# Performance work log

Measured on AMD Instinct MI355X. Metric: run time of the kernel, lower is better.

## Reference

```python
import jax, jax.numpy as jnp
import numpy as np

EPS = 1e-6
SIGMA = 0.02  # inverse-quadratic kernel scale (RGBuvHistBlock default)
H_BINS = 128


def _rgb_uv_hist(x, mu):
    # x: [B, 3, H, W] in [0, 1]; mu: [h] bin centers in [-3, 3]
    x = jnp.clip(x, 0.0, 1.0)
    B = x.shape[0]
    I = x.reshape(B, 3, -1)                       # [B, 3, N]
    Iy = jnp.sqrt(jnp.sum(I * I, axis=1) + EPS)   # [B, N] intensity scaling
    logI = jnp.log(I + EPS)                       # [B, 3, N]

    def kern(d):
        # inverse-quadratic kernel: 1 / (1 + (|d| / sigma)^2)
        return 1.0 / (1.0 + (d / SIGMA) ** 2)

    def chan(c0, c1, c2):
        Iu = logI[:, c0] - logI[:, c1]            # [B, N]
        Iv = logI[:, c0] - logI[:, c2]            # [B, N]
        du = kern(jnp.abs(Iu[:, :, None] - mu[None, None, :]))  # [B, N, h]
        dv = kern(jnp.abs(Iv[:, :, None] - mu[None, None, :]))  # [B, N, h]
        a = Iy[:, :, None] * du                   # [B, N, h]
        return jnp.einsum('bnu,bnv->buv', a, dv)  # [B, h, h]

    # channel order: r vs (g,b), g vs (r,b), b vs (r,g)
    hists = jnp.stack([chan(0, 1, 2), chan(1, 0, 2), chan(2, 0, 1)], axis=1)  # [B,3,h,h]
    norm = jnp.sum(hists, axis=(1, 2, 3)).reshape(-1, 1, 1, 1) + EPS
    return hists / norm


def setup_inputs() -> dict:
    key = jax.random.key(0)
    k1, k2 = jax.random.split(key)
    B, C, H, W = 4, 3, 256, 256
    pred = jax.random.uniform(k1, (B, C, H, W), dtype=jnp.float32)
    target = jax.random.uniform(k2, (B, C, H, W), dtype=jnp.float32)
    return {"pred": pred, "target": target}


def reference(pred, target):
    mu = jnp.linspace(-3.0, 3.0, H_BINS, dtype=pred.dtype)
    pred_hist = _rgb_uv_hist(pred, mu)
    target_hist = _rgb_uv_hist(target, mu)
    diff = jnp.sqrt(target_hist) - jnp.sqrt(pred_hist)
    return (1.0 / np.sqrt(2.0)) * jnp.sqrt(jnp.sum(diff * diff)) / pred_hist.shape[0]
```

## Files before the change

kernel.cpp:

```cpp
#include <hip/hip_runtime.h>

#define NPIX   65536
#define HB     128
#define EPSF   1e-6f
#define ROWB   80
#define MATB   (HB * ROWB)
#define BUFB   (3 * MATB)
#define PPW    24576
#define NCHUNK 32

typedef _Float16 half8  __attribute__((ext_vector_type(8)));
typedef __fp16   fp16x2 __attribute__((ext_vector_type(2)));
typedef float    f32x16 __attribute__((ext_vector_type(16)));
typedef float    f32x2  __attribute__((ext_vector_type(2)));

__device__ __forceinline__ unsigned pk2(float a, float b) {
    union { fp16x2 h; unsigned u; } cv;
    cv.h = __builtin_amdgcn_cvt_pkrtz(a, b);
    return cv.u;
}

__global__ __launch_bounds__(512, 2) void hist_mfma(
    const float* __restrict__ pred, const float* __restrict__ tgt,
    unsigned* __restrict__ parts, float* __restrict__ norms, int nchunk)
{
    __shared__ char smat[2 * BUFB];
    __shared__ float wsum[8];

    const int t    = threadIdx.x;
    const int lane = t & 63;
    const int wave = t >> 6;
    const int chunk = blockIdx.x % nchunk;
    const int ib    = blockIdx.x / nchunk;
    const int b     = ib & 3;
    const int img   = ib >> 2;
    const int kchunk = NPIX / nchunk;
    const int nreg   = kchunk >> 5;

    const float* __restrict__ base = (img ? tgt : pred) + (size_t)b * 3 * NPIX;
    const float* __restrict__ Rp = base;
    const float* __restrict__ Gp = base + NPIX;
    const float* __restrict__ Bp = base + 2 * NPIX;

    const int   i16     = t & 15;
    const int   rbase   = t >> 4;
    const float MU0     = (float)rbase * (300.0f / 127.0f) - 150.0f;
    const float MUSTEP  = 32.0f * (300.0f / 127.0f);
    char* genp0 = smat + rbase * ROWB + i16 * 4;
    char* genp1 = genp0 + BUFB;

    const int wu = wave >> 2;
    const int wv = wave & 3;
    const int la = lane & 31;

    f32x16 acc[3][2];
#pragma unroll
    for (int g = 0; g < 3; ++g)
#pragma unroll
        for (int i = 0; i < 2; ++i)
#pragma unroll
            for (int r = 0; r < 16; ++r) acc[g][i][r] = 0.0f;

    const int n0 = chunk * kchunk;

    f32x2 Ra, Ga, Ba, Rb, Gb, Bb;
    f32x2 ddrg, ddrb, ddgb, rw2;

    auto issue_ld = [&](int reg, f32x2& R, f32x2& G, f32x2& B) {
        const int n = n0 + reg * 32 + 2 * i16;
        R = *reinterpret_cast<const f32x2*>(Rp + n);
        G = *reinterpret_cast<const f32x2*>(Gp + n);
        B = *reinterpret_cast<const f32x2*>(Bp + n);
    };

    auto scalars = [&](f32x2 R, f32x2 G, f32x2 B) {
        const float C = 34.65735902799726547086f;
        float r0 = fminf(fmaxf(R.x, 0.0f), 1.0f);
        float r1 = fminf(fmaxf(R.y, 0.0f), 1.0f);
        float g0 = fminf(fmaxf(G.x, 0.0f), 1.0f);
        float g1 = fminf(fmaxf(G.y, 0.0f), 1.0f);
        float b0 = fminf(fmaxf(B.x, 0.0f), 1.0f);
        float b1 = fminf(fmaxf(B.y, 0.0f), 1.0f);
        float lr0 = __builtin_amdgcn_logf(r0 + EPSF);
        float lr1 = __builtin_amdgcn_logf(r1 + EPSF);
        float lg0 = __builtin_amdgcn_logf(g0 + EPSF);
        float lg1 = __builtin_amdgcn_logf(g1 + EPSF);
        float lb0 = __builtin_amdgcn_logf(b0 + EPSF);
        float lb1 = __builtin_amdgcn_logf(b1 + EPSF);
        ddrg.x = (lr0 - lg0) * C;  ddrg.y = (lr1 - lg1) * C;
        ddrb.x = (lr0 - lb0) * C;  ddrb.y = (lr1 - lb1) * C;
        ddgb.x = (lg0 - lb0) * C;  ddgb.y = (lg1 - lb1) * C;
        const float s0 = __builtin_fmaf(r0, r0,
                          __builtin_fmaf(g0, g0,
                           __builtin_fmaf(b0, b0, EPSF)));
        const float s1 = __builtin_fmaf(r1, r1,
                          __builtin_fmaf(g1, g1,
                           __builtin_fmaf(b1, b1, EPSF)));
        rw2.x = __builtin_amdgcn_sqrtf(__builtin_amdgcn_sqrtf(s0));
        rw2.y = __builtin_amdgcn_sqrtf(__builtin_amdgcn_sqrtf(s1));
    };

    auto gen_mat = [&](char* bp, int mat, f32x2 dd) {
        float m = MU0;
#pragma unroll
        for (int s = 0; s < 4; ++s) {
            const float ex = dd.x - m, ey = dd.y - m;
            const float tx = __builtin_fmaf(ex, ex, 1.0f);
            const float ty = __builtin_fmaf(ey, ey, 1.0f);
            const float vx = __builtin_amdgcn_rcpf(tx) * rw2.x;
            const float vy = __builtin_amdgcn_rcpf(ty) * rw2.y;
            *reinterpret_cast<unsigned*>(bp + mat * MATB + s * 32 * ROWB)
                = pk2(vx, vy);
            m += MUSTEP;
        }
    };

    auto rd = [&](const char* mp, int matid, int row, int koff) -> half8 {
        return *reinterpret_cast<const half8*>(mp + matid * MATB
                                               + row * ROWB + koff);
    };

    auto body = [&](const char* mp, char* gp, bool dogen) {
        const int kbase = (lane >> 5) << 4;
        const int r0 = wu * 64 + la;
        const int c0 = wv * 32 + la;

        if (dogen) gen_mat(gp, 0, ddrg);
        {
            half8 a0 = rd(mp, 0, r0,      kbase);
            half8 a1 = rd(mp, 0, r0 + 32, kbase);
            half8 p  = rd(mp, 1, c0,      kbase);
            __builtin_amdgcn_s_setprio(1);
            acc[0][0] = __builtin_amdgcn_mfma_f32_32x32x16_f16(a0, p, acc[0][0], 0, 0, 0);
            acc[0][1] = __builtin_amdgcn_mfma_f32_32x32x16_f16(a1, p, acc[0][1], 0, 0, 0);
            __builtin_amdgcn_s_setprio(0);

            if (dogen) gen_mat(gp, 1, ddrb);
            half8 q   = rd(mp, 2, c0,      kbase);
            half8 bb0 = rd(mp, 1, r0,      kbase);
            half8 bb1 = rd(mp, 1, r0 + 32, kbase);
            __builtin_amdgcn_s_setprio(1);
            acc[1][0] = __builtin_amdgcn_mfma_f32_32x32x16_f16(a0, q, acc[1][0], 0, 0, 0);
            acc[1][1] = __builtin_amdgcn_mfma_f32_32x32x16_f16(a1, q, acc[1][1], 0, 0, 0);
            acc[2][0] = __builtin_amdgcn_mfma_f32_32x32x16_f16(bb0, q, acc[2][0], 0, 0, 0);
            acc[2][1] = __builtin_amdgcn_mfma_f32_32x32x16_f16(bb1, q, acc[2][1], 0, 0, 0);
            __builtin_amdgcn_s_setprio(0);
        }

        if (dogen) gen_mat(gp, 2, ddgb);
        {
            const int k1 = 32 + kbase;
            half8 a0  = rd(mp, 0, r0,      k1);
            half8 a1  = rd(mp, 0, r0 + 32, k1);
            half8 p   = rd(mp, 1, c0,      k1);
            half8 q   = rd(mp, 2, c0,      k1);
            half8 bb0 = rd(mp, 1, r0,      k1);
            half8 bb1 = rd(mp, 1, r0 + 32, k1);
            __builtin_amdgcn_s_setprio(1);
            acc[0][0] = __builtin_amdgcn_mfma_f32_32x32x16_f16(a0, p, acc[0][0], 0, 0, 0);
            acc[0][1] = __builtin_amdgcn_mfma_f32_32x32x16_f16(a1, p, acc[0][1], 0, 0, 0);
            acc[1][0] = __builtin_amdgcn_mfma_f32_32x32x16_f16(a0, q, acc[1][0], 0, 0, 0);
            acc[1][1] = __builtin_amdgcn_mfma_f32_32x32x16_f16(a1, q, acc[1][1], 0, 0, 0);
            acc[2][0] = __builtin_amdgcn_mfma_f32_32x32x16_f16(bb0, q, acc[2][0], 0, 0, 0);
            acc[2][1] = __builtin_amdgcn_mfma_f32_32x32x16_f16(bb1, q, acc[2][1], 0, 0, 0);
            __builtin_amdgcn_s_setprio(0);
        }
    };

    issue_ld(0, Ra, Ga, Ba);
    scalars(Ra, Ga, Ba);
    gen_mat(genp0, 0, ddrg);
    gen_mat(genp0, 1, ddrb);
    gen_mat(genp0, 2, ddgb);
    issue_ld(1, Rb, Gb, Bb);
    __syncthreads();

    for (int rg = 0; rg < nreg; rg += 2) {
        scalars(Rb, Gb, Bb);
        issue_ld(min(rg + 2, nreg - 1), Ra, Ga, Ba);
        body(smat, genp1, true);
        __syncthreads();
        scalars(Ra, Ga, Ba);
        issue_ld(min(rg + 3, nreg - 1), Rb, Gb, Bb);
        body(smat + BUFB, genp0, rg + 2 < nreg);
        __syncthreads();
    }

    unsigned* pb0 = parts + (size_t)blockIdx.x * PPW;
    float blksum = 0.0f;
#pragma unroll
    for (int g = 0; g < 3; ++g)
#pragma unroll
        for (int i2 = 0; i2 < 2; ++i2) {
            unsigned* wp = pb0
                + (size_t)(((g * 8 + wave) * 2 + i2) * 8) * 64 + lane;
#pragma unroll
            for (int rh = 0; rh < 8; ++rh) {
                wp[rh * 64] = pk2(acc[g][i2][2 * rh], acc[g][i2][2 * rh + 1]);
                blksum += acc[g][i2][2 * rh] + acc[g][i2][2 * rh + 1];
            }
        }

    for (int o = 32; o > 0; o >>= 1) blksum += __shfl_down(blksum, o, 64);
    if (lane == 0) wsum[wave] = blksum;
    __syncthreads();
    if (t == 0) {
        float s = 0.0f;
#pragma unroll
        for (int w = 0; w < 8; ++w) s += wsum[w];
        atomicAdd(&norms[ib], s);
    }
}

__global__ __launch_bounds__(256) void reduce_loss(
    const unsigned* __restrict__ parts, const float* __restrict__ norms,
    float* __restrict__ acc, int nchunk)
{
    const int i      = blockIdx.x * 256 + threadIdx.x;
    const int comb12 = i >> 13;
    const int rest   = i & 8191;
    const int b      = comb12 / 3;
    const int g      = comb12 % 3;
    const unsigned* pp = parts + (size_t)(b * nchunk) * PPW + g * 8192 + rest;
    const unsigned* pt = parts + (size_t)((4 + b) * nchunk) * PPW + g * 8192 + rest;

    float hp0 = 0.0f, hp1 = 0.0f, ht0 = 0.0f, ht1 = 0.0f;
    int k = 0;
    for (; k + 8 <= nchunk; k += 8) {
#pragma unroll
        for (int j = 0; j < 8; ++j) {
            union { unsigned u; fp16x2 h; } a, c;
            a.u = pp[(size_t)(k + j) * PPW];
            c.u = pt[(size_t)(k + j) * PPW];
            hp0 += (float)a.h.x;  hp1 += (float)a.h.y;
            ht0 += (float)c.h.x;  ht1 += (float)c.h.y;
        }
    }
    for (; k < nchunk; ++k) {
        union { unsigned u; fp16x2 h; } a, c;
        a.u = pp[(size_t)k * PPW];
        c.u = pt[(size_t)k * PPW];
        hp0 += (float)a.h.x;  hp1 += (float)a.h.y;
        ht0 += (float)c.h.x;  ht1 += (float)c.h.y;
    }

    const float rp = __builtin_amdgcn_rcpf(norms[b] + EPSF);
    const float rt = __builtin_amdgcn_rcpf(norms[4 + b] + EPSF);
    const float d0 = __builtin_amdgcn_sqrtf(ht0 * rt)
                   - __builtin_amdgcn_sqrtf(hp0 * rp);
    const float d1 = __builtin_amdgcn_sqrtf(ht1 * rt)
                   - __builtin_amdgcn_sqrtf(hp1 * rp);
    float s = __builtin_fmaf(d0, d0, d1 * d1);
    for (int o = 32; o > 0; o >>= 1) s += __shfl_down(s, o, 64);
    __shared__ float wsum[4];
    if ((threadIdx.x & 63) == 0) wsum[threadIdx.x >> 6] = s;
    __syncthreads();
    if (threadIdx.x == 0) atomicAdd(acc, wsum[0] + wsum[1] + wsum[2] + wsum[3]);
}

__global__ void final_k(const float* __restrict__ acc, float* __restrict__ out)
{
    out[0] = __builtin_amdgcn_sqrtf(acc[0]) * 0.70710678118654752440f * 0.25f;
}

extern "C" void kernel_launch(void* const* d_in, const int* in_sizes, int n_in,
                              void* d_out, int out_size, void* d_ws, size_t ws_size,
                              hipStream_t stream)
{
    const float* pred = (const float*)d_in[0];
    const float* tgt  = (const float*)d_in[1];
    float* ws  = (float*)d_ws;
    float* out = (float*)d_out;

    float*    norms = ws;
    float*    acc   = ws + 8;
    unsigned* parts = (unsigned*)(ws + 16);

    int nchunk = NCHUNK;
    while (nchunk > 1) {
        const size_t need = (16 + (size_t)8 * nchunk * PPW) * sizeof(float);
        if (need <= ws_size) break;
        nchunk >>= 1;
    }

    (void)hipMemsetAsync(ws, 0, 9 * sizeof(float), stream);

    hist_mfma<<<8 * nchunk, 512, 0, stream>>>(pred, tgt, parts, norms, nchunk);
    reduce_loss<<<12 * 8192 / 256, 256, 0, stream>>>(parts, norms, acc, nchunk);
    final_k<<<1, 1, 0, stream>>>(acc, out);
}
```

Baseline: 100.9 us.

## Split work across 12 waves with one histogram per wave group

The block grows from 512 to 768 threads. Each group of 256 threads now generates only one of the three kernel matrices, and each group of four waves computes a full 128x128 histogram as 2x2 tiles of 64x64. Each thread takes two log calls instead of six and writes eight rows instead of twelve, and every wave issues four MFMAs per k-step with plain A/B fragment reuse. The cost is more waves per block, a different register budget under launch_bounds(768,3), and a new output layout in the partial buffer that the reduce kernel must still index correctly.

```diff
diff --git a/kernel.cpp b/kernel.cpp
--- a/kernel.cpp
+++ b/kernel.cpp
@@ -20,12 +20,12 @@
     return cv.u;
 }
 
-__global__ __launch_bounds__(512, 2) void hist_mfma(
+__global__ __launch_bounds__(768, 3) void hist_mfma(
     const float* __restrict__ pred, const float* __restrict__ tgt,
     unsigned* __restrict__ parts, float* __restrict__ norms, int nchunk)
 {
     __shared__ char smat[2 * BUFB];
-    __shared__ float wsum[8];
+    __shared__ float wsum[12];
 
     const int t    = threadIdx.x;
     const int lane = t & 63;
@@ -42,29 +42,35 @@
     const float* __restrict__ Gp = base + NPIX;
     const float* __restrict__ Bp = base + 2 * NPIX;
 
-    const int   i16     = t & 15;
-    const int   rbase   = t >> 4;
+    const int   mat     = t >> 8;
+    const int   tp      = t & 255;
+    const int   i16     = tp & 15;
+    const int   rbase   = tp >> 4;
     const float MU0     = (float)rbase * (300.0f / 127.0f) - 150.0f;
-    const float MUSTEP  = 32.0f * (300.0f / 127.0f);
-    char* genp0 = smat + rbase * ROWB + i16 * 4;
+    const float MUSTEP  = 16.0f * (300.0f / 127.0f);
+    char* genp0 = smat + mat * MATB + rbase * ROWB + i16 * 4;
     char* genp1 = genp0 + BUFB;
 
-    const int wu = wave >> 2;
-    const int wv = wave & 3;
-    const int la = lane & 31;
-
-    f32x16 acc[3][2];
-#pragma unroll
-    for (int g = 0; g < 3; ++g)
-#pragma unroll
-        for (int i = 0; i < 2; ++i)
-#pragma unroll
-            for (int r = 0; r < 16; ++r) acc[g][i][r] = 0.0f;
+    const int g    = wave >> 2;
+    const int i2   = (wave >> 1) & 1;
+    const int j2   = wave & 1;
+    const int Amat = (g == 2) ? 1 : 0;
+    const int Bmat = (g == 0) ? 1 : 2;
+    const int la   = lane & 31;
+    const int kb16 = (lane >> 5) << 4;
+    const int arow = i2 * 64 + la;
+    const int brow = j2 * 64 + la;
+
+    f32x16 acc[4];
+#pragma unroll
+    for (int i = 0; i < 4; ++i)
+#pragma unroll
+        for (int r = 0; r < 16; ++r) acc[i][r] = 0.0f;
 
     const int n0 = chunk * kchunk;
 
     f32x2 Ra, Ga, Ba, Rb, Gb, Bb;
-    f32x2 ddrg, ddrb, ddgb, rw2;
+    f32x2 dd, rw2;
 
     auto issue_ld = [&](int reg, f32x2& R, f32x2& G, f32x2& B) {
         const int n = n0 + reg * 32 + 2 * i16;
@@ -81,15 +87,14 @@
         float g1 = fminf(fmaxf(G.y, 0.0f), 1.0f);
         float b0 = fminf(fmaxf(B.x, 0.0f), 1.0f);
         float b1 = fminf(fmaxf(B.y, 0.0f), 1.0f);
-        float lr0 = __builtin_amdgcn_logf(r0 + EPSF);
-        float lr1 = __builtin_amdgcn_logf(r1 + EPSF);
-        float lg0 = __builtin_amdgcn_logf(g0 + EPSF);
-        float lg1 = __builtin_amdgcn_logf(g1 + EPSF);
-        float lb0 = __builtin_amdgcn_logf(b0 + EPSF);
-        float lb1 = __builtin_amdgcn_logf(b1 + EPSF);
-        ddrg.x = (lr0 - lg0) * C;  ddrg.y = (lr1 - lg1) * C;
-        ddrb.x = (lr0 - lb0) * C;  ddrb.y = (lr1 - lb1) * C;
-        ddgb.x = (lg0 - lb0) * C;  ddgb.y = (lg1 - lb1) * C;
+        const float x0a = (mat == 2) ? g0 : r0;
+        const float x1a = (mat == 2) ? g1 : r1;
+        const float y0a = (mat == 0) ? g0 : b0;
+        const float y1a = (mat == 0) ? g1 : b1;
+        dd.x = (__builtin_amdgcn_logf(x0a + EPSF)
+              - __builtin_amdgcn_logf(y0a + EPSF)) * C;
+        dd.y = (__builtin_amdgcn_logf(x1a + EPSF)
+              - __builtin_amdgcn_logf(y1a + EPSF)) * C;
         const float s0 = __builtin_fmaf(r0, r0,
                           __builtin_fmaf(g0, g0,
                            __builtin_fmaf(b0, b0, EPSF)));
@@ -100,106 +105,69 @@
         rw2.y = __builtin_amdgcn_sqrtf(__builtin_amdgcn_sqrtf(s1));
     };
 
-    auto gen_mat = [&](char* bp, int mat, f32x2 dd) {
+    auto gen = [&](char* bp) {
         float m = MU0;
 #pragma unroll
-        for (int s = 0; s < 4; ++s) {
+        for (int s = 0; s < 8; ++s) {
             const float ex = dd.x - m, ey = dd.y - m;
             const float tx = __builtin_fmaf(ex, ex, 1.0f);
             const float ty = __builtin_fmaf(ey, ey, 1.0f);
             const float vx = __builtin_amdgcn_rcpf(tx) * rw2.x;
             const float vy = __builtin_amdgcn_rcpf(ty) * rw2.y;
-            *reinterpret_cast<unsigned*>(bp + mat * MATB + s * 32 * ROWB)
-                = pk2(vx, vy);
+            *reinterpret_cast<unsigned*>(bp + s * 16 * ROWB) = pk2(vx, vy);
             m += MUSTEP;
         }
     };
 
-    auto rd = [&](const char* mp, int matid, int row, int koff) -> half8 {
-        return *reinterpret_cast<const half8*>(mp + matid * MATB
-                                               + row * ROWB + koff);
-    };
-
-    auto body = [&](const char* mp, char* gp, bool dogen) {
-        const int kbase = (lane >> 5) << 4;
-        const int r0 = wu * 64 + la;
-        const int c0 = wv * 32 + la;
-
-        if (dogen) gen_mat(gp, 0, ddrg);
-        {
-            half8 a0 = rd(mp, 0, r0,      kbase);
-            half8 a1 = rd(mp, 0, r0 + 32, kbase);
-            half8 p  = rd(mp, 1, c0,      kbase);
+    auto do_mfma = [&](const char* mp) {
+        const char* Ab = mp + Amat * MATB;
+        const char* Bb = mp + Bmat * MATB;
+#pragma unroll
+        for (int kb = 0; kb < 2; ++kb) {
+            const int koff = kb * 32 + kb16;
+            half8 a0 = *reinterpret_cast<const half8*>(Ab + arow * ROWB + koff);
+            half8 a1 = *reinterpret_cast<const half8*>(Ab + (arow + 32) * ROWB + koff);
+            half8 b0 = *reinterpret_cast<const half8*>(Bb + brow * ROWB + koff);
+            half8 b1 = *reinterpret_cast<const half8*>(Bb + (brow + 32) * ROWB + koff);
             __builtin_amdgcn_s_setprio(1);
-            acc[0][0] = __builtin_amdgcn_mfma_f32_32x32x16_f16(a0, p, acc[0][0], 0, 0, 0);
-            acc[0][1] = __builtin_amdgcn_mfma_f32_32x32x16_f16(a1, p, acc[0][1], 0, 0, 0);
-            __builtin_amdgcn_s_setprio(0);
-
-            if (dogen) gen_mat(gp, 1, ddrb);
-            half8 q   = rd(mp, 2, c0,      kbase);
-            half8 bb0 = rd(mp, 1, r0,      kbase);
-            half8 bb1 = rd(mp, 1, r0 + 32, kbase);
-            __builtin_amdgcn_s_setprio(1);
-            acc[1][0] = __builtin_amdgcn_mfma_f32_32x32x16_f16(a0, q, acc[1][0], 0, 0, 0);
-            acc[1][1] = __builtin_amdgcn_mfma_f32_32x32x16_f16(a1, q, acc[1][1], 0, 0, 0);
-            acc[2][0] = __builtin_amdgcn_mfma_f32_32x32x16_f16(bb0, q, acc[2][0], 0, 0, 0);
-            acc[2][1] = __builtin_amdgcn_mfma_f32_32x32x16_f16(bb1, q, acc[2][1], 0, 0, 0);
-            __builtin_amdgcn_s_setprio(0);
-        }
-
-        if (dogen) gen_mat(gp, 2, ddgb);
-        {
-            const int k1 = 32 + kbase;
-            half8 a0  = rd(mp, 0, r0,      k1);
-            half8 a1  = rd(mp, 0, r0 + 32, k1);
-            half8 p   = rd(mp, 1, c0,      k1);
-            half8 q   = rd(mp, 2, c0,      k1);
-            half8 bb0 = rd(mp, 1, r0,      k1);
-            half8 bb1 = rd(mp, 1, r0 + 32, k1);
-            __builtin_amdgcn_s_setprio(1);
-            acc[0][0] = __builtin_amdgcn_mfma_f32_32x32x16_f16(a0, p, acc[0][0], 0, 0, 0);
-            acc[0][1] = __builtin_amdgcn_mfma_f32_32x32x16_f16(a1, p, acc[0][1], 0, 0, 0);
-            acc[1][0] = __builtin_amdgcn_mfma_f32_32x32x16_f16(a0, q, acc[1][0], 0, 0, 0);
-            acc[1][1] = __builtin_amdgcn_mfma_f32_32x32x16_f16(a1, q, acc[1][1], 0, 0, 0);
-            acc[2][0] = __builtin_amdgcn_mfma_f32_32x32x16_f16(bb0, q, acc[2][0], 0, 0, 0);
-            acc[2][1] = __builtin_amdgcn_mfma_f32_32x32x16_f16(bb1, q, acc[2][1], 0, 0, 0);
+            acc[0] = __builtin_amdgcn_mfma_f32_32x32x16_f16(a0, b0, acc[0], 0, 0, 0);
+            acc[1] = __builtin_amdgcn_mfma_f32_32x32x16_f16(a0, b1, acc[1], 0, 0, 0);
+            acc[2] = __builtin_amdgcn_mfma_f32_32x32x16_f16(a1, b0, acc[2], 0, 0, 0);
+            acc[3] = __builtin_amdgcn_mfma_f32_32x32x16_f16(a1, b1, acc[3], 0, 0, 0);
             __builtin_amdgcn_s_setprio(0);
         }
     };
 
     issue_ld(0, Ra, Ga, Ba);
     scalars(Ra, Ga, Ba);
-    gen_mat(genp0, 0, ddrg);
-    gen_mat(genp0, 1, ddrb);
-    gen_mat(genp0, 2, ddgb);
+    gen(genp0);
     issue_ld(1, Rb, Gb, Bb);
     __syncthreads();
 
     for (int rg = 0; rg < nreg; rg += 2) {
         scalars(Rb, Gb, Bb);
         issue_ld(min(rg + 2, nreg - 1), Ra, Ga, Ba);
-        body(smat, genp1, true);
+        gen(genp1);
+        do_mfma(smat);
         __syncthreads();
         scalars(Ra, Ga, Ba);
         issue_ld(min(rg + 3, nreg - 1), Rb, Gb, Bb);
-        body(smat + BUFB, genp0, rg + 2 < nreg);
+        if (rg + 2 < nreg) gen(genp0);
+        do_mfma(smat + BUFB);
         __syncthreads();
     }
 
     unsigned* pb0 = parts + (size_t)blockIdx.x * PPW;
     float blksum = 0.0f;
 #pragma unroll
-    for (int g = 0; g < 3; ++g)
-#pragma unroll
-        for (int i2 = 0; i2 < 2; ++i2) {
-            unsigned* wp = pb0
-                + (size_t)(((g * 8 + wave) * 2 + i2) * 8) * 64 + lane;
-#pragma unroll
-            for (int rh = 0; rh < 8; ++rh) {
-                wp[rh * 64] = pk2(acc[g][i2][2 * rh], acc[g][i2][2 * rh + 1]);
-                blksum += acc[g][i2][2 * rh] + acc[g][i2][2 * rh + 1];
-            }
-        }
+    for (int idx = 0; idx < 4; ++idx) {
+        unsigned* wp = pb0 + (size_t)((wave * 4 + idx) * 8) * 64 + lane;
+#pragma unroll
+        for (int rh = 0; rh < 8; ++rh) {
+            wp[rh * 64] = pk2(acc[idx][2 * rh], acc[idx][2 * rh + 1]);
+            blksum += acc[idx][2 * rh] + acc[idx][2 * rh + 1];
+        }
+    }
 
     for (int o = 32; o > 0; o >>= 1) blksum += __shfl_down(blksum, o, 64);
     if (lane == 0) wsum[wave] = blksum;
@@ -207,7 +175,7 @@
     if (t == 0) {
         float s = 0.0f;
 #pragma unroll
-        for (int w = 0; w < 8; ++w) s += wsum[w];
+        for (int w = 0; w < 12; ++w) s += wsum[w];
         atomicAdd(&norms[ib], s);
     }
 }
@@ -285,7 +253,7 @@
 
     (void)hipMemsetAsync(ws, 0, 9 * sizeof(float), stream);
 
-    hist_mfma<<<8 * nchunk, 512, 0, stream>>>(pred, tgt, parts, norms, nchunk);
+    hist_mfma<<<8 * nchunk, 768, 0, stream>>>(pred, tgt, parts, norms, nchunk);
     reduce_loss<<<12 * 8192 / 256, 256, 0, stream>>>(parts, norms, acc, nchunk);
     final_k<<<1, 1, 0, stream>>>(acc, out);
 }
```

After: 105.1 us. +4.2%, slower.
